# Optimization experiments

Hardware: AMD Instinct MI355X
Metric: run time of the kernel (lower is better)

The kernel has to match this reference:

```python
import jax, jax.numpy as jnp
import numpy as np

EPS = 1e-5

def _layernorm(x, g, b):
    mu = jnp.mean(x, axis=-1, keepdims=True)
    var = jnp.mean(jnp.square(x - mu), axis=-1, keepdims=True)
    return (x - mu) * jax.lax.rsqrt(var + EPS) * g + b

def setup_inputs() -> dict:
    key = jax.random.key(0)
    ks = jax.random.split(key, 12)
    B, S, D, F = 2, 2048, 1024, 4096
    w = lambda k, shp: jax.random.normal(k, shp, dtype=jnp.float32) * 0.02
    return {
        "x":  jax.random.normal(ks[0], (B, S, D), dtype=jnp.float32),
        "Wq": w(ks[1], (D, D)), "bq": jnp.zeros((D,), jnp.float32),
        "Wk": w(ks[2], (D, D)), "bk": jnp.zeros((D,), jnp.float32),
        "Wv": w(ks[3], (D, D)), "bv": jnp.zeros((D,), jnp.float32),
        "W1": w(ks[4], (F, D)), "b1": jnp.zeros((F,), jnp.float32),
        "W2": w(ks[5], (D, F)), "b2": jnp.zeros((D,), jnp.float32),
        "g1": jnp.ones((D,), jnp.float32), "beta1": jnp.zeros((D,), jnp.float32),
        "g2": jnp.ones((D,), jnp.float32), "beta2": jnp.zeros((D,), jnp.float32),
    }

def reference(x, Wq, bq, Wk, bk, Wv, bv, W1, b1, W2, b2, g1, beta1, g2, beta2):
    B, S, D = x.shape
    H = 16
    dk = D // H
    # QKV projections (torch nn.Linear: y = x @ W.T + b)
    q = (x @ Wq.T + bq).reshape(B, S, H, dk).transpose(0, 2, 1, 3)  # [B,H,S,dk]
    k = (x @ Wk.T + bk).reshape(B, S, H, dk).transpose(0, 2, 1, 3)
    v = (x @ Wv.T + bv).reshape(B, S, H, dk).transpose(0, 2, 1, 3)
    # naive full attention (no mask, dropout=identity in eval)
    scores = jnp.einsum("bhqd,bhkd->bhqk", q, k) / jnp.sqrt(jnp.float32(dk))
    probs = jax.nn.softmax(scores, axis=-1)
    attn = jnp.einsum("bhqk,bhkd->bhqd", probs, v)  # [B,H,S,dk]
    attn_out = attn.transpose(0, 2, 1, 3).reshape(B, S, D)  # NOTE: no output proj (combine unused in source)
    # residual + LN1
    h = _layernorm(x + attn_out, g1, beta1)
    # FFN: linear2(relu(linear1(h)))
    ffn = jax.nn.relu(h @ W1.T + b1) @ W2.T + b2
    # residual + LN2
    return _layernorm(h + ffn, g2, beta2)
```

## Files before the change

### kernel.cpp

```cpp
#include <hip/hip_runtime.h>
#include <stdint.h>

typedef unsigned short u16;
typedef __bf16 bf16x8 __attribute__((ext_vector_type(8)));
typedef short s16x8 __attribute__((ext_vector_type(8)));
typedef float f32x4 __attribute__((ext_vector_type(4)));

union FragU { s16x8 s; bf16x8 b; uint4 u; };

__device__ __forceinline__ f32x4 mfma_bf16(s16x8 a, s16x8 b, f32x4 c) {
    FragU ua, ub; ua.s = a; ub.s = b;
    return __builtin_amdgcn_mfma_f32_16x16x32_bf16(ua.b, ub.b, c, 0, 0, 0);
}

__device__ __forceinline__ u16 f2bf(float f) {
    uint32_t u = __float_as_uint(f);
    u += 0x7fffu + ((u >> 16) & 1u);
    return (u16)(u >> 16);
}

__device__ __forceinline__ float bf2f(u16 u) {
    return __uint_as_float((uint32_t)u << 16);
}

__device__ __forceinline__ void gload_lds16(const void* g, void* l) {
    __builtin_amdgcn_global_load_lds((__attribute__((address_space(1))) void*)g,
                                     (__attribute__((address_space(3))) void*)l,
                                     16, 0, 0);
}

__device__ __forceinline__ void xcd_swz(int& bx, int& by, int& bz) {
    int nx = gridDim.x, ny = gridDim.y;
    int nwg = nx * ny * gridDim.z;
    int lin = blockIdx.x + nx * (blockIdx.y + ny * blockIdx.z);
    int cpx = nwg >> 3;
    int s = (lin & 7) * cpx + (lin >> 3);
    bx = s % nx; s /= nx;
    by = s % ny; bz = s / ny;
}

__global__ void k_cast_all(
    const float* __restrict__ s0, u16* __restrict__ d0, int n0,
    const float* __restrict__ s1, u16* __restrict__ d1, int n1,
    const float* __restrict__ s2, u16* __restrict__ d2, int n2,
    const float* __restrict__ s3, u16* __restrict__ d3, int n3,
    const float* __restrict__ s4, u16* __restrict__ d4, int n4_,
    const float* __restrict__ s5, u16* __restrict__ d5, int n5)
{
    const float* src; u16* dst; int n4;
    switch (blockIdx.y) {
        case 0: src = s0; dst = d0; n4 = n0; break;
        case 1: src = s1; dst = d1; n4 = n1; break;
        case 2: src = s2; dst = d2; n4 = n2; break;
        case 3: src = s3; dst = d3; n4 = n3; break;
        case 4: src = s4; dst = d4; n4 = n4_; break;
        default: src = s5; dst = d5; n4 = n5; break;
    }
    int i = blockIdx.x * blockDim.x + threadIdx.x;
    int stride = gridDim.x * blockDim.x;
    for (; i < n4; i += stride) {
        float4 v = ((const float4*)src)[i];
        u16 us[4] = {f2bf(v.x), f2bf(v.y), f2bf(v.z), f2bf(v.w)};
        *(uint2*)(dst + (size_t)i * 4) = *(uint2*)us;
    }
}

template<int RELU, int OUTMODE>
__device__ __forceinline__ void gemm_body(
    u16* __restrict__ As, u16* __restrict__ Bs,
    const u16* __restrict__ A, const u16* __restrict__ W,
    const float* __restrict__ bias, void* __restrict__ Cout,
    int M, int N, int K, int row0, int col0, int kbeg, int kend)
{
    const int tid  = threadIdx.x;
    const int wid  = tid >> 6;
    const int lane = tid & 63;
    const int g    = lane >> 4;
    const int cc   = lane & 15;
    const int wr   = wid >> 1;
    const int wc   = wid & 1;

    f32x4 zero = {0.f, 0.f, 0.f, 0.f};
    f32x4 acc[4][4];
#pragma unroll
    for (int i = 0; i < 4; i++)
#pragma unroll
        for (int j = 0; j < 4; j++) acc[i][j] = zero;

    const int srow = tid >> 3;
    const int scol = ((tid & 7) ^ (srow & 7)) * 8;
    const u16* gA0 = A + (size_t)(row0 + srow) * K + scol;
    const u16* gB0 = W + (size_t)(col0 + srow) * K + scol;
    u16* lA0 = &As[wid * 512];
    u16* lB0 = &Bs[wid * 512];

    const int xm = (cc & 7);

    for (int k0 = kbeg; k0 < kend; k0 += 64) {
#pragma unroll
        for (int j = 0; j < 4; j++)
            gload_lds16(gA0 + (size_t)(j * 32) * K + k0, lA0 + j * 2048);
#pragma unroll
        for (int j = 0; j < 4; j++)
            gload_lds16(gB0 + (size_t)(j * 32) * K + k0, lB0 + j * 2048);
        __syncthreads();

#pragma unroll
        for (int h = 0; h < 2; h++) {
            const int slot = ((h * 4 + g) ^ xm) * 8;
            s16x8 af[4], bf[4];
#pragma unroll
            for (int mi = 0; mi < 4; mi++)
                af[mi] = *(const s16x8*)&As[(wr * 64 + mi * 16 + cc) * 64 + slot];
#pragma unroll
            for (int ni = 0; ni < 4; ni++)
                bf[ni] = *(const s16x8*)&Bs[(wc * 64 + ni * 16 + cc) * 64 + slot];
#pragma unroll
            for (int mi = 0; mi < 4; mi++)
#pragma unroll
                for (int ni = 0; ni < 4; ni++)
                    acc[mi][ni] = mfma_bf16(af[mi], bf[ni], acc[mi][ni]);
        }
        __syncthreads();
    }

#pragma unroll
    for (int ni = 0; ni < 4; ni++) {
        int col = col0 + wc * 64 + ni * 16 + cc;
        float bvv = 0.f;
        if (OUTMODE != 2) bvv = bias[col];
        if (OUTMODE == 3) {
            int head = col >> 6, dh = col & 63;
#pragma unroll
            for (int mi = 0; mi < 4; mi++) {
                int row = row0 + wr * 64 + mi * 16 + g * 4;
                int bb = row >> 11, sl = row & 2047;
                u16 us[4];
#pragma unroll
                for (int r = 0; r < 4; r++) us[r] = f2bf(acc[mi][ni][r] + bvv);
                *(uint2*)&((u16*)Cout)[(((size_t)(bb * 16 + head) * 64 + dh) << 11) + sl]
                    = *(uint2*)us;
            }
        } else {
#pragma unroll
            for (int mi = 0; mi < 4; mi++) {
                int row = row0 + wr * 64 + mi * 16 + g * 4;
#pragma unroll
                for (int r = 0; r < 4; r++) {
                    float v = acc[mi][ni][r] + bvv;
                    if (RELU) v = fmaxf(v, 0.f);
                    size_t idx = (size_t)(row + r) * N + col;
                    if (OUTMODE == 0) ((float*)Cout)[idx] = v;
                    else              ((u16*)Cout)[idx] = f2bf(v);
                }
            }
        }
    }
}

#define GEMM_LDS_DECL \
    __shared__ __align__(16) u16 As[128 * 64]; \
    __shared__ __align__(16) u16 Bs[128 * 64];

__global__ __launch_bounds__(256, 4) void k_gemm_qkv(
    const u16* __restrict__ A, const u16* __restrict__ Wq, const u16* __restrict__ Wk,
    const u16* __restrict__ Wv, const float* __restrict__ bq, const float* __restrict__ bk,
    const float* __restrict__ bv, u16* __restrict__ Q, u16* __restrict__ K,
    u16* __restrict__ Vt, int M, int N, int Kd)
{
    GEMM_LDS_DECL
    int bx, by, bz; xcd_swz(bx, by, bz);
    if (bz == 0)
        gemm_body<0, 1>(As, Bs, A, Wq, bq, Q,  M, N, Kd, by * 128, bx * 128, 0, Kd);
    else if (bz == 1)
        gemm_body<0, 1>(As, Bs, A, Wk, bk, K,  M, N, Kd, by * 128, bx * 128, 0, Kd);
    else
        gemm_body<0, 3>(As, Bs, A, Wv, bv, Vt, M, N, Kd, by * 128, bx * 128, 0, Kd);
}

__global__ __launch_bounds__(256, 4) void k_gemm_relu_bf16(
    const u16* __restrict__ A, const u16* __restrict__ W, const float* __restrict__ bias,
    u16* __restrict__ C, int M, int N, int K)
{
    GEMM_LDS_DECL
    int bx, by, bz; xcd_swz(bx, by, bz);
    gemm_body<1, 1>(As, Bs, A, W, bias, C, M, N, K, by * 128, bx * 128, 0, K);
}

__global__ __launch_bounds__(256, 4) void k_gemm_part(
    const u16* __restrict__ A, const u16* __restrict__ W,
    u16* __restrict__ p0, u16* __restrict__ p1, u16* __restrict__ p2, u16* __restrict__ p3,
    int M, int N, int K)
{
    GEMM_LDS_DECL
    int bx, by, bz; xcd_swz(bx, by, bz);
    u16* out = (bz == 0) ? p0 : (bz == 1) ? p1 : (bz == 2) ? p2 : p3;
    gemm_body<0, 2>(As, Bs, A, W, nullptr, out, M, N, K, by * 128, bx * 128, bz * 1024, bz * 1024 + 1024);
}

__global__ __launch_bounds__(512, 4) void k_flash(
    const u16* __restrict__ Q, const u16* __restrict__ Kb,
    const u16* __restrict__ Vt, u16* __restrict__ O)
{
    constexpr int S = 2048, Dm = 1024, H = 16;
    constexpr int KVB = 128, NT = S / KVB;
    constexpr float qsc = 0.125f * 1.44269504f;
    int bx, by, bz; xcd_swz(bx, by, bz);
    int qt = bx, h = by, b = bz;
    int tid = threadIdx.x, wid = tid >> 6, lane = tid & 63;
    int g = lane >> 4, cc = lane & 15;

    __shared__ __align__(16) u16 Ks[2][128 * 64];
    __shared__ __align__(16) u16 Vs[64 * 128];

    int q0 = qt * 128 + wid * 16;
    size_t base = (size_t)b * S * Dm + h * 64;

    FragU uq0, uq1, qs0, qs1;
    uq0.s = *(const s16x8*)(Q + base + (size_t)(q0 + cc) * Dm + g * 8);
    uq1.s = *(const s16x8*)(Q + base + (size_t)(q0 + cc) * Dm + 32 + g * 8);
#pragma unroll
    for (int e = 0; e < 8; e++) {
        qs0.b[e] = (__bf16)((float)uq0.b[e] * qsc);
        qs1.b[e] = (__bf16)((float)uq1.b[e] * qsc);
    }
    s16x8 qf0 = qs0.s, qf1 = qs1.s;

    f32x4 minit = {-8.f, -8.f, -8.f, -8.f};
    f32x4 zero = {0.f, 0.f, 0.f, 0.f};
    f32x4 o[4];
#pragma unroll
    for (int t = 0; t < 4; t++) o[t] = zero;
    f32x4 lacc = zero;

    const int krow = tid >> 3;
    const int kcol = ((tid & 7) ^ (krow & 7)) * 8;
    const u16* kSrcBase = Kb + base + (size_t)krow * Dm + kcol;
    const int kOff = wid * 512;

    const int vrow = tid >> 3;
    const int vch  = (tid & 7) * 8;
    const int xmv  = (vrow & 7) << 3;
    const int cb0  = ((vch >> 5) << 5) | (((vch >> 4) & 1) << 2) | (((vch >> 2) & 3) << 3);
    const int cb1  = cb0 + 64;
    const u16* vSrcBase = Vt + (size_t)(b * H + h) * 64 * S + (size_t)vrow * S;
    u16* vq0a = &Vs[(vrow * 128 + cb0) ^ xmv];
    u16* vq0b = &Vs[(vrow * 128 + cb0 + 8) ^ xmv];
    u16* vq1a = &Vs[(vrow * 128 + cb1) ^ xmv];
    u16* vq1b = &Vs[(vrow * 128 + cb1 + 8) ^ xmv];

    const int xm = cc & 7;

    gload_lds16(kSrcBase,                   &Ks[0][kOff]);
    gload_lds16(kSrcBase + (size_t)64 * Dm, &Ks[0][kOff + 4096]);
    __builtin_amdgcn_sched_barrier(0);
    s16x8 vpre0 = *(const s16x8*)(vSrcBase + vch);
    s16x8 vpre1 = *(const s16x8*)(vSrcBase + 64 + vch);
    __builtin_amdgcn_sched_barrier(0);

    for (int it = 0; it < NT; ++it) {
        const int cur = it & 1;
        const int kv0 = it * KVB;

        asm volatile("s_waitcnt vmcnt(2)" ::: "memory");
        __builtin_amdgcn_s_barrier();
        __builtin_amdgcn_sched_barrier(0);

        {
            FragU a0, a1; a0.s = vpre0; a1.s = vpre1;
            *(uint2*)vq0a = make_uint2(a0.u.x, a0.u.y);
            *(uint2*)vq0b = make_uint2(a0.u.z, a0.u.w);
            *(uint2*)vq1a = make_uint2(a1.u.x, a1.u.y);
            *(uint2*)vq1b = make_uint2(a1.u.z, a1.u.w);
        }
        __builtin_amdgcn_sched_barrier(0);
        if (it + 1 < NT) {
            gload_lds16(kSrcBase + (size_t)(kv0 + KVB) * Dm,      &Ks[cur ^ 1][kOff]);
            gload_lds16(kSrcBase + (size_t)(kv0 + KVB + 64) * Dm, &Ks[cur ^ 1][kOff + 4096]);
        }
        __builtin_amdgcn_sched_barrier(0);
        asm volatile("s_waitcnt lgkmcnt(0)" ::: "memory");
        __builtin_amdgcn_s_barrier();
        __builtin_amdgcn_sched_barrier(0);

        const u16* Kc = Ks[cur];
        f32x4 sacc[8];
#pragma unroll
        for (int t = 0; t < 8; t++) sacc[t] = minit;
        __builtin_amdgcn_s_setprio(1);
#pragma unroll
        for (int t = 0; t < 8; t++) {
            const u16* kr = &Kc[(t * 16 + cc) * 64];
            s16x8 kf0 = *(const s16x8*)(kr + ((0 + g) ^ xm) * 8);
            s16x8 kf1 = *(const s16x8*)(kr + ((4 + g) ^ xm) * 8);
            sacc[t] = mfma_bf16(kf0, qf0, sacc[t]);
            sacc[t] = mfma_bf16(kf1, qf1, sacc[t]);
        }
        __builtin_amdgcn_s_setprio(0);

        FragU pb[4];
#pragma unroll
        for (int t = 0; t < 8; t++)
#pragma unroll
            for (int r = 0; r < 4; r++) {
                float pv = __builtin_amdgcn_exp2f(sacc[t][r]);
                lacc[r] += pv;
                pb[t >> 1].b[(t & 1) * 4 + r] = (__bf16)pv;
            }

        __builtin_amdgcn_s_setprio(1);
#pragma unroll
        for (int td = 0; td < 4; td++) {
            const int rb = (td * 16 + cc) * 128;
#pragma unroll
            for (int kk = 0; kk < 4; kk++) {
                s16x8 vf = *(const s16x8*)&Vs[(rb + kk * 32 + g * 8) ^ (xm << 3)];
                o[td] = mfma_bf16(vf, pb[kk].s, o[td]);
            }
        }
        __builtin_amdgcn_s_setprio(0);

        if (it + 1 < NT) {
            vpre0 = *(const s16x8*)(vSrcBase + kv0 + KVB + vch);
            vpre1 = *(const s16x8*)(vSrcBase + kv0 + KVB + 64 + vch);
        }
        __builtin_amdgcn_sched_barrier(0);
    }

    float l_run = (lacc[0] + lacc[1]) + (lacc[2] + lacc[3]);
    l_run += __shfl_xor(l_run, 16, 64);
    l_run += __shfl_xor(l_run, 32, 64);
    float inv = 1.f / l_run;
#pragma unroll
    for (int td = 0; td < 4; td++) {
        u16 us[4] = {f2bf(o[td][0] * inv), f2bf(o[td][1] * inv),
                     f2bf(o[td][2] * inv), f2bf(o[td][3] * inv)};
        *(uint2*)&O[(size_t)(b * S + q0 + cc) * Dm + h * 64 + td * 16 + g * 4] = *(uint2*)us;
    }
}

__global__ __launch_bounds__(256) void k_ln1(
    const float* __restrict__ A, const u16* __restrict__ B,
    const float* __restrict__ gw, const float* __restrict__ bw,
    u16* __restrict__ outb)
{
    constexpr int D = 1024;
    int row = blockIdx.x;
    int t = threadIdx.x;
    int lane = t & 63, wid = t >> 6;
    size_t idx = (size_t)row * D + t * 4;
    float4 va = ((const float4*)(A + (size_t)row * D))[t];
    uint2 vb = *(const uint2*)(B + idx);
    float v0 = va.x + bf2f((u16)vb.x);
    float v1 = va.y + bf2f((u16)(vb.x >> 16));
    float v2 = va.z + bf2f((u16)vb.y);
    float v3 = va.w + bf2f((u16)(vb.y >> 16));
    float sum = v0 + v1 + v2 + v3;
    float sq  = v0 * v0 + v1 * v1 + v2 * v2 + v3 * v3;
#pragma unroll
    for (int off = 1; off < 64; off <<= 1) {
        sum += __shfl_xor(sum, off, 64);
        sq  += __shfl_xor(sq,  off, 64);
    }
    __shared__ float s1[4], s2[4];
    if (lane == 0) { s1[wid] = sum; s2[wid] = sq; }
    __syncthreads();
    sum = s1[0] + s1[1] + s1[2] + s1[3];
    sq  = s2[0] + s2[1] + s2[2] + s2[3];
    float mu  = sum * (1.f / D);
    float var = sq * (1.f / D) - mu * mu;
    float rs  = rsqrtf(var + 1e-5f);
    float4 gv = ((const float4*)gw)[t];
    float4 bv = ((const float4*)bw)[t];
    u16 us[4] = {f2bf((v0 - mu) * rs * gv.x + bv.x),
                 f2bf((v1 - mu) * rs * gv.y + bv.y),
                 f2bf((v2 - mu) * rs * gv.z + bv.z),
                 f2bf((v3 - mu) * rs * gv.w + bv.w)};
    *(uint2*)(outb + idx) = *(uint2*)us;
}

__global__ __launch_bounds__(256) void k_ln2(
    const u16* __restrict__ A,
    const u16* __restrict__ p0, const u16* __restrict__ p1,
    const u16* __restrict__ p2, const u16* __restrict__ p3,
    const float* __restrict__ bias,
    const float* __restrict__ gw, const float* __restrict__ bw,
    float* __restrict__ outf)
{
    constexpr int D = 1024;
    int row = blockIdx.x;
    int t = threadIdx.x;
    int lane = t & 63, wid = t >> 6;
    size_t idx = (size_t)row * D + t * 4;
    uint2 ha = *(const uint2*)(A + idx);
    float4 bb = ((const float4*)bias)[t];
    float v0 = bf2f((u16)ha.x)         + bb.x;
    float v1 = bf2f((u16)(ha.x >> 16)) + bb.y;
    float v2 = bf2f((u16)ha.y)         + bb.z;
    float v3 = bf2f((u16)(ha.y >> 16)) + bb.w;
    const u16* ps[4] = {p0, p1, p2, p3};
#pragma unroll
    for (int pi = 0; pi < 4; pi++) {
        uint2 q = *(const uint2*)(ps[pi] + idx);
        v0 += bf2f((u16)q.x);
        v1 += bf2f((u16)(q.x >> 16));
        v2 += bf2f((u16)q.y);
        v3 += bf2f((u16)(q.y >> 16));
    }
    float sum = v0 + v1 + v2 + v3;
    float sq  = v0 * v0 + v1 * v1 + v2 * v2 + v3 * v3;
#pragma unroll
    for (int off = 1; off < 64; off <<= 1) {
        sum += __shfl_xor(sum, off, 64);
        sq  += __shfl_xor(sq,  off, 64);
    }
    __shared__ float s1[4], s2[4];
    if (lane == 0) { s1[wid] = sum; s2[wid] = sq; }
    __syncthreads();
    sum = s1[0] + s1[1] + s1[2] + s1[3];
    sq  = s2[0] + s2[1] + s2[2] + s2[3];
    float mu  = sum * (1.f / D);
    float var = sq * (1.f / D) - mu * mu;
    float rs  = rsqrtf(var + 1e-5f);
    float4 gv = ((const float4*)gw)[t];
    float4 bv = ((const float4*)bw)[t];
    float4 yo = {(v0 - mu) * rs * gv.x + bv.x,
                 (v1 - mu) * rs * gv.y + bv.y,
                 (v2 - mu) * rs * gv.z + bv.z,
                 (v3 - mu) * rs * gv.w + bv.w};
    ((float4*)(outf + (size_t)row * D))[t] = yo;
}

extern "C" void kernel_launch(void* const* d_in, const int* in_sizes, int n_in,
                              void* d_out, int out_size, void* d_ws, size_t ws_size,
                              hipStream_t stream)
{
    constexpr int B = 2, S = 2048, D = 1024, F = 4096, H = 16;
    constexpr int M = B * S;
    const float* x   = (const float*)d_in[0];
    const float* Wq  = (const float*)d_in[1];
    const float* bq  = (const float*)d_in[2];
    const float* Wk  = (const float*)d_in[3];
    const float* bk  = (const float*)d_in[4];
    const float* Wv  = (const float*)d_in[5];
    const float* bv  = (const float*)d_in[6];
    const float* W1  = (const float*)d_in[7];
    const float* b1  = (const float*)d_in[8];
    const float* W2  = (const float*)d_in[9];
    const float* b2  = (const float*)d_in[10];
    const float* g1  = (const float*)d_in[11];
    const float* be1 = (const float*)d_in[12];
    const float* g2  = (const float*)d_in[13];
    const float* be2 = (const float*)d_in[14];
    float* out = (float*)d_out;

    char* ws = (char*)d_ws;
    size_t off = 0;
    auto alloc = [&](size_t bytes) {
        void* p = ws + off;
        off += (bytes + 255) & ~(size_t)255;
        return p;
    };
    u16* xb    = (u16*)alloc((size_t)M * D * 2);
    u16* wqb   = (u16*)alloc((size_t)D * D * 2);
    u16* wkb   = (u16*)alloc((size_t)D * D * 2);
    u16* wvb   = (u16*)alloc((size_t)D * D * 2);
    u16* w1b   = (u16*)alloc((size_t)F * D * 2);
    u16* w2b   = (u16*)alloc((size_t)D * F * 2);
    u16* Qb    = (u16*)alloc((size_t)M * D * 2);
    u16* Kbf   = (u16*)alloc((size_t)M * D * 2);
    u16* Vtb   = (u16*)alloc((size_t)M * D * 2);
    u16* ffn1  = (u16*)alloc((size_t)M * F * 2);
    u16* attnb = (u16*)alloc((size_t)M * D * 2);
    u16* hb    = (u16*)alloc((size_t)M * D * 2);
    u16* p0 = xb;
    u16* p1 = w1b;
    u16* p2 = attnb;
    u16* p3 = Qb;

    dim3 blk(256);
    k_cast_all<<<dim3(128, 6), blk, 0, stream>>>(
        x,  xb,  M * D / 4,
        Wq, wqb, D * D / 4,
        Wk, wkb, D * D / 4,
        Wv, wvb, D * D / 4,
        W1, w1b, F * D / 4,
        W2, w2b, D * F / 4);

    k_gemm_qkv<<<dim3(D / 128, M / 128, 3), blk, 0, stream>>>(
        xb, wqb, wkb, wvb, bq, bk, bv, Qb, Kbf, Vtb, M, D, D);
    k_flash<<<dim3(S / 128, H, B), dim3(512), 0, stream>>>(Qb, Kbf, Vtb, attnb);
    k_ln1<<<dim3(M), blk, 0, stream>>>(x, attnb, g1, be1, hb);
    k_gemm_relu_bf16<<<dim3(F / 128, M / 128), blk, 0, stream>>>(hb, w1b, b1, ffn1, M, F, D);
    k_gemm_part<<<dim3(D / 128, M / 128, 4), blk, 0, stream>>>(
        ffn1, w2b, p0, p1, p2, p3, M, D, F);
    k_ln2<<<dim3(M), blk, 0, stream>>>(hb, p0, p1, p2, p3, b2, g2, be2, out);
}
```

Before: 186.5 us.

## Double-buffer GEMM LDS tiles with BK=32 and async prefetch of next k-step

The shared GEMM body now uses two LDS buffers with a 32-wide k-step instead of one 64-wide buffer. It prefetches the next tile via direct global-to-LDS loads while computing the current one, waiting only on older vmcnt. It also raises wave priority around the MFMA block. The aim is to hide global load latency behind compute. The cost is twice as many loop iterations and barriers, plus a narrower swizzle that may change LDS bank conflicts.

```diff
diff --git a/kernel.cpp b/kernel.cpp
--- a/kernel.cpp
+++ b/kernel.cpp
@@ -67,7 +67,7 @@
 
 template<int RELU, int OUTMODE>
 __device__ __forceinline__ void gemm_body(
-    u16* __restrict__ As, u16* __restrict__ Bs,
+    u16* __restrict__ AsB, u16* __restrict__ BsB,
     const u16* __restrict__ A, const u16* __restrict__ W,
     const float* __restrict__ bias, void* __restrict__ Cout,
     int M, int N, int K, int row0, int col0, int kbeg, int kend)
@@ -87,41 +87,60 @@
 #pragma unroll
         for (int j = 0; j < 4; j++) acc[i][j] = zero;
 
-    const int srow = tid >> 3;
-    const int scol = ((tid & 7) ^ (srow & 7)) * 8;
+    const int srow = tid >> 2;
+    const int scol = ((tid & 3) ^ (srow & 3)) * 8;
     const u16* gA0 = A + (size_t)(row0 + srow) * K + scol;
     const u16* gB0 = W + (size_t)(col0 + srow) * K + scol;
-    u16* lA0 = &As[wid * 512];
-    u16* lB0 = &Bs[wid * 512];
-
-    const int xm = (cc & 7);
-
-    for (int k0 = kbeg; k0 < kend; k0 += 64) {
-#pragma unroll
-        for (int j = 0; j < 4; j++)
-            gload_lds16(gA0 + (size_t)(j * 32) * K + k0, lA0 + j * 2048);
-#pragma unroll
-        for (int j = 0; j < 4; j++)
-            gload_lds16(gB0 + (size_t)(j * 32) * K + k0, lB0 + j * 2048);
-        __syncthreads();
-
-#pragma unroll
-        for (int h = 0; h < 2; h++) {
-            const int slot = ((h * 4 + g) ^ xm) * 8;
-            s16x8 af[4], bf[4];
-#pragma unroll
-            for (int mi = 0; mi < 4; mi++)
-                af[mi] = *(const s16x8*)&As[(wr * 64 + mi * 16 + cc) * 64 + slot];
+    const int ldOff = wid * 512;
+
+    const int xm = (cc & 3);
+
+    auto stage = [&](int buf, int k0) {
+        u16* lA = AsB + buf * 4096 + ldOff;
+        u16* lB = BsB + buf * 4096 + ldOff;
+        gload_lds16(gA0 + k0,                  lA);
+        gload_lds16(gA0 + (size_t)64 * K + k0, lA + 2048);
+        gload_lds16(gB0 + k0,                  lB);
+        gload_lds16(gB0 + (size_t)64 * K + k0, lB + 2048);
+    };
+
+    const int nsteps = (kend - kbeg) >> 5;
+    stage(0, kbeg);
+    __builtin_amdgcn_sched_barrier(0);
+
+    for (int step = 0; step < nsteps; ++step) {
+        const int cur = step & 1;
+        if (step + 1 < nsteps) {
+            stage(cur ^ 1, kbeg + (step + 1) * 32);
+            __builtin_amdgcn_sched_barrier(0);
+            asm volatile("s_waitcnt vmcnt(4)" ::: "memory");
+        } else {
+            asm volatile("s_waitcnt vmcnt(0)" ::: "memory");
+        }
+        __builtin_amdgcn_s_barrier();
+        __builtin_amdgcn_sched_barrier(0);
+
+        const u16* Asc = AsB + cur * 4096;
+        const u16* Bsc = BsB + cur * 4096;
+        const int slot = (g ^ xm) * 8;
+        s16x8 af[4], bf[4];
+#pragma unroll
+        for (int mi = 0; mi < 4; mi++)
+            af[mi] = *(const s16x8*)&Asc[(wr * 64 + mi * 16 + cc) * 32 + slot];
+#pragma unroll
+        for (int ni = 0; ni < 4; ni++)
+            bf[ni] = *(const s16x8*)&Bsc[(wc * 64 + ni * 16 + cc) * 32 + slot];
+        __builtin_amdgcn_s_setprio(1);
+#pragma unroll
+        for (int mi = 0; mi < 4; mi++)
 #pragma unroll
             for (int ni = 0; ni < 4; ni++)
-                bf[ni] = *(const s16x8*)&Bs[(wc * 64 + ni * 16 + cc) * 64 + slot];
-#pragma unroll
-            for (int mi = 0; mi < 4; mi++)
-#pragma unroll
-                for (int ni = 0; ni < 4; ni++)
-                    acc[mi][ni] = mfma_bf16(af[mi], bf[ni], acc[mi][ni]);
-        }
-        __syncthreads();
+                acc[mi][ni] = mfma_bf16(af[mi], bf[ni], acc[mi][ni]);
+        __builtin_amdgcn_s_setprio(0);
+
+        __builtin_amdgcn_sched_barrier(0);
+        __builtin_amdgcn_s_barrier();
+        __builtin_amdgcn_sched_barrier(0);
     }
 
 #pragma unroll
@@ -159,8 +178,8 @@
 }
 
 #define GEMM_LDS_DECL \
-    __shared__ __align__(16) u16 As[128 * 64]; \
-    __shared__ __align__(16) u16 Bs[128 * 64];
+    __shared__ __align__(16) u16 As[2][128 * 32]; \
+    __shared__ __align__(16) u16 Bs[2][128 * 32];
 
 __global__ __launch_bounds__(256, 4) void k_gemm_qkv(
     const u16* __restrict__ A, const u16* __restrict__ Wq, const u16* __restrict__ Wk,
@@ -171,11 +190,11 @@
     GEMM_LDS_DECL
     int bx, by, bz; xcd_swz(bx, by, bz);
     if (bz == 0)
-        gemm_body<0, 1>(As, Bs, A, Wq, bq, Q,  M, N, Kd, by * 128, bx * 128, 0, Kd);
+        gemm_body<0, 1>(&As[0][0], &Bs[0][0], A, Wq, bq, Q,  M, N, Kd, by * 128, bx * 128, 0, Kd);
     else if (bz == 1)
-        gemm_body<0, 1>(As, Bs, A, Wk, bk, K,  M, N, Kd, by * 128, bx * 128, 0, Kd);
+        gemm_body<0, 1>(&As[0][0], &Bs[0][0], A, Wk, bk, K,  M, N, Kd, by * 128, bx * 128, 0, Kd);
     else
-        gemm_body<0, 3>(As, Bs, A, Wv, bv, Vt, M, N, Kd, by * 128, bx * 128, 0, Kd);
+        gemm_body<0, 3>(&As[0][0], &Bs[0][0], A, Wv, bv, Vt, M, N, Kd, by * 128, bx * 128, 0, Kd);
 }
 
 __global__ __launch_bounds__(256, 4) void k_gemm_relu_bf16(
@@ -184,7 +203,7 @@
 {
     GEMM_LDS_DECL
     int bx, by, bz; xcd_swz(bx, by, bz);
-    gemm_body<1, 1>(As, Bs, A, W, bias, C, M, N, K, by * 128, bx * 128, 0, K);
+    gemm_body<1, 1>(&As[0][0], &Bs[0][0], A, W, bias, C, M, N, K, by * 128, bx * 128, 0, K);
 }
 
 __global__ __launch_bounds__(256, 4) void k_gemm_part(
@@ -195,7 +214,8 @@
     GEMM_LDS_DECL
     int bx, by, bz; xcd_swz(bx, by, bz);
     u16* out = (bz == 0) ? p0 : (bz == 1) ? p1 : (bz == 2) ? p2 : p3;
-    gemm_body<0, 2>(As, Bs, A, W, nullptr, out, M, N, K, by * 128, bx * 128, bz * 1024, bz * 1024 + 1024);
+    gemm_body<0, 2>(&As[0][0], &Bs[0][0], A, W, nullptr, out, M, N, K, by * 128, bx * 128,
+                    bz * 1024, bz * 1024 + 1024);
 }
 
 __global__ __launch_bounds__(512, 4) void k_flash(
```

Result: slower. 198.2 us (+6.3%).
